# Optimization experiments

Hardware: AMD Instinct MI355X
Metric: run time of the kernel (lower is better)

## Reference

```python
import jax, jax.numpy as jnp
import numpy as np

N = 50000      # total nodes (actors) across batch
E = 300000     # edges surviving the distance threshold
N_AGT = 128    # n_actor
N_CTX = 128    # n_ctx == n_actor for A2A
EPS = 1e-5


def _gn(x, gamma, beta):
    # torch GroupNorm(num_groups=1) on a [N, C] tensor: normalize over C per row
    mu = jnp.mean(x, axis=-1, keepdims=True)
    var = jnp.mean((x - mu) ** 2, axis=-1, keepdims=True)
    return (x - mu) * jax.lax.rsqrt(var + EPS) * gamma + beta


def setup_inputs() -> dict:
    key = jax.random.key(0)
    ks = jax.random.split(key, 16)
    s = 0.02
    f32 = jnp.float32
    inp = {
        'agts': jax.random.normal(ks[0], (N, N_AGT), f32),
        'ctx': jax.random.normal(ks[1], (N, N_CTX), f32),
        'agt_ctrs': jax.random.normal(ks[2], (N, 2), f32),
        'ctx_ctrs': jax.random.normal(ks[3], (N, 2), f32),
        'hi': jax.random.randint(ks[4], (E,), 0, N, dtype=jnp.int32),
        'wi': jax.random.randint(ks[5], (E,), 0, N, dtype=jnp.int32),
        # dist: nn.Linear(2, n_ctx) -> ReLU -> Linear(n_ctx, n_ctx, GN, act)
        'w_d1': jax.random.normal(ks[6], (N_CTX, 2), f32) * s,
        'b_d1': jnp.zeros((N_CTX,), f32),
        'w_d2': jax.random.normal(ks[7], (N_CTX, N_CTX), f32) * s,
        'g_d2': jnp.ones((N_CTX,), f32), 'bt_d2': jnp.zeros((N_CTX,), f32),
        # query: Linear(n_agt, n_ctx, GN, act)
        'w_q': jax.random.normal(ks[8], (N_CTX, N_AGT), f32) * s,
        'g_q': jnp.ones((N_CTX,), f32), 'bt_q': jnp.zeros((N_CTX,), f32),
        # ctx: Linear(3*n_ctx, n_agt, GN, act) -> nn.Linear(n_agt, n_agt, bias=False)
        'w_c1': jax.random.normal(ks[9], (N_AGT, 3 * N_CTX), f32) * s,
        'g_c1': jnp.ones((N_AGT,), f32), 'bt_c1': jnp.zeros((N_AGT,), f32),
        'w_c2': jax.random.normal(ks[10], (N_AGT, N_AGT), f32) * s,
        # agt: nn.Linear(n_agt, n_agt, bias=False)
        'w_a': jax.random.normal(ks[11], (N_AGT, N_AGT), f32) * s,
        # norm: GroupNorm(1, n_agt)
        'g_n': jnp.ones((N_AGT,), f32), 'bt_n': jnp.zeros((N_AGT,), f32),
        # linear: Linear(n_agt, n_agt, GN, act=False)
        'w_l': jax.random.normal(ks[12], (N_AGT, N_AGT), f32) * s,
        'g_l': jnp.ones((N_AGT,), f32), 'bt_l': jnp.zeros((N_AGT,), f32),
    }
    return inp


def reference(agts, ctx, agt_ctrs, ctx_ctrs, hi, wi,
              w_d1, b_d1, w_d2, g_d2, bt_d2,
              w_q, g_q, bt_q,
              w_c1, g_c1, bt_c1, w_c2,
              w_a, g_n, bt_n,
              w_l, g_l, bt_l):
    res = agts
    # edge-wise distance features: [E, 2] -> [E, n_ctx]
    d = agt_ctrs[hi] - ctx_ctrs[wi]
    d = jax.nn.relu(d @ w_d1.T + b_d1)
    d = jax.nn.relu(_gn(d @ w_d2.T, g_d2, bt_d2))
    # edge-wise query from gathered target nodes: [E, n_ctx]
    q = jax.nn.relu(_gn(agts[hi] @ w_q.T, g_q, bt_q))
    # fuse dist/query/context: [E, 3*n_ctx] -> [E, n_agt]
    e = jnp.concatenate([d, q, ctx[wi]], axis=-1)
    e = jax.nn.relu(_gn(e @ w_c1.T, g_c1, bt_c1))
    e = e @ w_c2.T
    # scatter-add messages back to nodes
    out = agts @ w_a.T
    out = out.at[hi].add(e)
    out = jax.nn.relu(_gn(out, g_n, bt_n))
    out = _gn(out @ w_l.T, g_l, bt_l)
    return jax.nn.relu(out + res)
```

## Files before the change

### kernel.cpp

```cpp
#include <hip/hip_runtime.h>
#include <hip/hip_bf16.h>

#define NCH 128
#define EB  32
#define NB  32

typedef __attribute__((ext_vector_type(8))) short bf16x8;
typedef __attribute__((ext_vector_type(4))) float f32x4;

__device__ inline unsigned short f2bf(float v) {
    __hip_bfloat16 h = __float2bfloat16(v);
    return __builtin_bit_cast(unsigned short, h);
}
__device__ inline float bf2f(unsigned short u) {
    return __builtin_bit_cast(float, (unsigned int)u << 16);
}

__device__ inline bf16x8 cvt8(const float* __restrict__ p) {
    bf16x8 r;
#pragma unroll
    for (int i = 0; i < 8; ++i) r[i] = (short)f2bf(p[i]);
    return r;
}

template<bool BF>
__device__ inline bf16x8 load_row8(const void* __restrict__ src, int node, int koff) {
    if constexpr (BF)
        return *(const bf16x8*)((const unsigned short*)src + (size_t)node * NCH + koff);
    else
        return cvt8((const float*)src + (size_t)node * NCH + koff);
}

__global__ __launch_bounds__(256) void convert_weights_kernel(
    const float* __restrict__ w_d2, const float* __restrict__ w_q,
    const float* __restrict__ w_c1, const float* __restrict__ w_c2,
    const float* __restrict__ w_a,  const float* __restrict__ w_l,
    unsigned short* __restrict__ out)
{
    int i = blockIdx.x * 256 + threadIdx.x;
    if (i >= 131072) return;
    const float* src; int off;
    if      (i < 16384)  { src = w_d2; off = i; }
    else if (i < 32768)  { src = w_q;  off = i - 16384; }
    else if (i < 49152)  { int j = i - 32768; src = w_c1; off = (j >> 7) * 384 + (j & 127); }
    else if (i < 65536)  { int j = i - 49152; src = w_c1; off = (j >> 7) * 384 + 128 + (j & 127); }
    else if (i < 81920)  { int j = i - 65536; src = w_c1; off = (j >> 7) * 384 + 256 + (j & 127); }
    else if (i < 98304)  { src = w_c2; off = i - 81920; }
    else if (i < 114688) { src = w_a;  off = i - 98304; }
    else                 { src = w_l;  off = i - 114688; }
    out[i] = f2bf(src[off]);
}

__device__ inline void gemm_k128_lds(const unsigned short* __restrict__ A,
                                     const unsigned short* __restrict__ W,
                                     int lane, int wave, f32x4 (&acc)[2][2])
{
#pragma unroll
    for (int k = 0; k < 4; ++k) {
        const int koff = k * 32 + (lane >> 4) * 8;
        bf16x8 a[2], b[2];
#pragma unroll
        for (int m = 0; m < 2; ++m) {
            int r = m * 16 + (lane & 15);
            int byte = (r * 256 + koff * 2) ^ ((r & 7) << 4);
            a[m] = *(const bf16x8*)((const char*)A + byte);
        }
#pragma unroll
        for (int n = 0; n < 2; ++n) {
            int wr = wave * 32 + n * 16 + (lane & 15);
            b[n] = *(const bf16x8*)(W + (size_t)wr * NCH + koff);
        }
#pragma unroll
        for (int m = 0; m < 2; ++m)
#pragma unroll
            for (int n = 0; n < 2; ++n)
                acc[m][n] = __builtin_amdgcn_mfma_f32_16x16x32_bf16(a[m], b[n], acc[m][n], 0, 0, 0);
    }
}

__device__ inline void gn_frag_stats(const f32x4 (&acc)[2][2],
                                     float (*red_s)[4], float (*red_q)[4],
                                     int t, float (&mu)[2][4], float (&rs)[2][4])
{
    const int lane = t & 63, wave = t >> 6;
    float s[2][4], q[2][4];
#pragma unroll
    for (int m = 0; m < 2; ++m)
#pragma unroll
        for (int j = 0; j < 4; ++j) {
            float sv = acc[m][0][j] + acc[m][1][j];
            float qv = acc[m][0][j] * acc[m][0][j] + acc[m][1][j] * acc[m][1][j];
#pragma unroll
            for (int off = 1; off < 16; off <<= 1) {
                sv += __shfl_xor(sv, off);
                qv += __shfl_xor(qv, off);
            }
            s[m][j] = sv; q[m][j] = qv;
        }
    if ((lane & 15) == 0) {
        const int rg = lane >> 4;
#pragma unroll
        for (int m = 0; m < 2; ++m)
#pragma unroll
            for (int j = 0; j < 4; ++j) {
                int r = m * 16 + rg * 4 + j;
                red_s[r][wave] = s[m][j];
                red_q[r][wave] = q[m][j];
            }
    }
    __syncthreads();
#pragma unroll
    for (int m = 0; m < 2; ++m)
#pragma unroll
        for (int j = 0; j < 4; ++j) {
            int r = m * 16 + ((lane >> 4) << 2) + j;
            float4 sv = *(const float4*)red_s[r];
            float4 qv = *(const float4*)red_q[r];
            float ssum = (sv.x + sv.y) + (sv.z + sv.w);
            float qsum = (qv.x + qv.y) + (qv.z + qv.w);
            float m_  = ssum * (1.f / NCH);
            float var = qsum * (1.f / NCH) - m_ * m_;
            mu[m][j] = m_;
            rs[m][j] = rsqrtf(var + 1e-5f);
        }
}

__device__ inline void gn_pack_store(const f32x4 (&acc)[2][2],
                                     const float (&mu)[2][4], const float (&rs)[2][4],
                                     const float* __restrict__ gamma,
                                     const float* __restrict__ beta,
                                     unsigned short* __restrict__ dst, int t)
{
    const int lane = t & 63, wave = t >> 6;
    const int c0 = wave * 32 + (lane & 15);
    const float g0 = gamma[c0],      b0 = beta[c0];
    const float g1 = gamma[c0 + 16], b1 = beta[c0 + 16];
#pragma unroll
    for (int m = 0; m < 2; ++m)
#pragma unroll
        for (int j = 0; j < 4; ++j) {
            int r = m * 16 + ((lane >> 4) << 2) + j;
            float v0 = fmaxf((acc[m][0][j] - mu[m][j]) * rs[m][j] * g0 + b0, 0.f);
            float v1 = fmaxf((acc[m][1][j] - mu[m][j]) * rs[m][j] * g1 + b1, 0.f);
            unsigned int p0 = f2bf(v0), p1 = f2bf(v1);
            unsigned int o0 = (unsigned int)__shfl_xor((int)p0, 1);
            unsigned int o1 = (unsigned int)__shfl_xor((int)p1, 1);
            if (!(lane & 1)) {
                int cb = c0 * 2;
                int byte0 = (r * 256 + cb) ^ ((r & 7) << 4);
                int byte1 = (r * 256 + cb + 32) ^ ((r & 7) << 4);
                *(unsigned int*)((char*)dst + byte0) = (p0 & 0xffffu) | (o0 << 16);
                *(unsigned int*)((char*)dst + byte1) = (p1 & 0xffffu) | (o1 << 16);
            }
        }
    __syncthreads();
}

__device__ inline void frag_pack_global(const f32x4 (&acc)[2][2],
                                        unsigned short* __restrict__ dst,
                                        int n0, int N, int t)
{
    const int lane = t & 63, wave = t >> 6;
    const int c0 = wave * 32 + (lane & 15);
#pragma unroll
    for (int m = 0; m < 2; ++m)
#pragma unroll
        for (int j = 0; j < 4; ++j) {
            int r = m * 16 + ((lane >> 4) << 2) + j;
            int ng = n0 + r;
            unsigned int p0 = f2bf(acc[m][0][j]);
            unsigned int p1 = f2bf(acc[m][1][j]);
            unsigned int o0 = (unsigned int)__shfl_xor((int)p0, 1);
            unsigned int o1 = (unsigned int)__shfl_xor((int)p1, 1);
            if (!(lane & 1) && ng < N) {
                unsigned int* rowp = (unsigned int*)(dst + (size_t)ng * NCH);
                rowp[c0 >> 1]        = (p0 & 0xffffu) | (o0 << 16);
                rowp[(c0 + 16) >> 1] = (p1 & 0xffffu) | (o1 << 16);
            }
        }
}

__global__ __launch_bounds__(256) void node_prep_kernel(
    const float* __restrict__ agts, const float* __restrict__ ctx,
    const unsigned short* __restrict__ wbf,
    const float* __restrict__ g_q, const float* __restrict__ bt_q,
    float* __restrict__ outbuf,
    unsigned short* __restrict__ pq, unsigned short* __restrict__ px, int N)
{
    const int t = threadIdx.x;
    const int lane = t & 63, wave = t >> 6;
    const int n0 = blockIdx.x * NB;

    __shared__ unsigned short bfQ[NB * NCH];
    __shared__ __align__(16) float red_s[NB][4];
    __shared__ __align__(16) float red_q[NB][4];

    const unsigned short* Wq   = wbf + 16384;
    const unsigned short* Wc1q = wbf + 49152;
    const unsigned short* Wc1x = wbf + 65536;
    const unsigned short* Wa   = wbf + 98304;

    int r0 = n0 + (lane & 15);      if (r0 >= N) r0 = N - 1;
    int r1 = n0 + 16 + (lane & 15); if (r1 >= N) r1 = N - 1;

    const f32x4 z = { 0.f, 0.f, 0.f, 0.f };
    f32x4 accO[2][2] = { { z, z }, { z, z } };
    f32x4 accQ[2][2] = { { z, z }, { z, z } };
#pragma unroll
    for (int k = 0; k < 4; ++k) {
        const int koff = k * 32 + (lane >> 4) * 8;
        bf16x8 a[2], bo[2], bq[2];
        a[0] = load_row8<false>(agts, r0, koff);
        a[1] = load_row8<false>(agts, r1, koff);
#pragma unroll
        for (int n = 0; n < 2; ++n) {
            int wr = wave * 32 + n * 16 + (lane & 15);
            bo[n] = *(const bf16x8*)(Wa + (size_t)wr * NCH + koff);
            bq[n] = *(const bf16x8*)(Wq + (size_t)wr * NCH + koff);
        }
#pragma unroll
        for (int m = 0; m < 2; ++m)
#pragma unroll
            for (int n = 0; n < 2; ++n) {
                accO[m][n] = __builtin_amdgcn_mfma_f32_16x16x32_bf16(a[m], bo[n], accO[m][n], 0, 0, 0);
                accQ[m][n] = __builtin_amdgcn_mfma_f32_16x16x32_bf16(a[m], bq[n], accQ[m][n], 0, 0, 0);
            }
    }
#pragma unroll
    for (int m = 0; m < 2; ++m)
#pragma unroll
        for (int n = 0; n < 2; ++n)
#pragma unroll
            for (int j = 0; j < 4; ++j) {
                int r = m * 16 + ((lane >> 4) << 2) + j;
                int ng = n0 + r;
                if (ng < N)
                    outbuf[(size_t)ng * NCH + wave * 32 + n * 16 + (lane & 15)] = accO[m][n][j];
            }
    float mu[2][4], rs[2][4];
    gn_frag_stats(accQ, red_s, red_q, t, mu, rs);
    gn_pack_store(accQ, mu, rs, g_q, bt_q, bfQ, t);

    f32x4 accPq[2][2] = { { z, z }, { z, z } };
    f32x4 accPx[2][2] = { { z, z }, { z, z } };
#pragma unroll
    for (int k = 0; k < 4; ++k) {
        const int koff = k * 32 + (lane >> 4) * 8;
        bf16x8 aq[2], ax[2], bq2[2], bx[2];
#pragma unroll
        for (int m = 0; m < 2; ++m) {
            int r = m * 16 + (lane & 15);
            int byte = (r * 256 + koff * 2) ^ ((r & 7) << 4);
            aq[m] = *(const bf16x8*)((const char*)bfQ + byte);
        }
        ax[0] = load_row8<false>(ctx, r0, koff);
        ax[1] = load_row8<false>(ctx, r1, koff);
#pragma unroll
        for (int n = 0; n < 2; ++n) {
            int wr = wave * 32 + n * 16 + (lane & 15);
            bq2[n] = *(const bf16x8*)(Wc1q + (size_t)wr * NCH + koff);
            bx[n]  = *(const bf16x8*)(Wc1x + (size_t)wr * NCH + koff);
        }
#pragma unroll
        for (int m = 0; m < 2; ++m)
#pragma unroll
            for (int n = 0; n < 2; ++n) {
                accPq[m][n] = __builtin_amdgcn_mfma_f32_16x16x32_bf16(aq[m], bq2[n], accPq[m][n], 0, 0, 0);
                accPx[m][n] = __builtin_amdgcn_mfma_f32_16x16x32_bf16(ax[m], bx[n], accPx[m][n], 0, 0, 0);
            }
    }
    frag_pack_global(accPq, pq, n0, N, t);
    frag_pack_global(accPx, px, n0, N, t);
}

__global__ __launch_bounds__(256) void edge_kernel_pre(
    const unsigned short* __restrict__ pq, const unsigned short* __restrict__ px,
    const float* __restrict__ agt_ctrs, const float* __restrict__ ctx_ctrs,
    const int* __restrict__ hi, const int* __restrict__ wi,
    const float* __restrict__ w_d1, const float* __restrict__ b_d1,
    const float* __restrict__ g_d2, const float* __restrict__ bt_d2,
    const float* __restrict__ g_c1, const float* __restrict__ bt_c1,
    const unsigned short* __restrict__ wbf,
    float* __restrict__ outbuf, int E)
{
    const int t = threadIdx.x;
    const int lane = t & 63;
    const int wave = t >> 6;
    const int e0 = blockIdx.x * EB;

    __shared__ unsigned short bfD[EB * NCH];
    __shared__ float S[EB][NCH + 4];
    __shared__ __align__(16) float red_s[EB][4];
    __shared__ __align__(16) float red_q[EB][4];
    __shared__ int   sh_h[EB], sh_w[EB];
    __shared__ float sh_dx[EB], sh_dy[EB];

    const unsigned short* Wd2  = wbf;
    const unsigned short* Wc1d = wbf + 32768;
    const unsigned short* Wc2  = wbf + 81920;

    if (t < EB) {
        int e = e0 + t; if (e >= E) e = E - 1;
        int h = hi[e], w = wi[e];
        sh_h[t] = h; sh_w[t] = w;
        sh_dx[t] = agt_ctrs[2 * h]     - ctx_ctrs[2 * w];
        sh_dy[t] = agt_ctrs[2 * h + 1] - ctx_ctrs[2 * w + 1];
    }
    __syncthreads();

    {
        const int r  = t >> 3;
        const int cc = t & 7;
        const int h = sh_h[r], w = sh_w[r];
#pragma unroll
        for (int half = 0; half < 2; ++half) {
            int c8 = (cc + half * 8) * 8;
            bf16x8 aq = load_row8<true>(pq, h, c8);
            bf16x8 ax = load_row8<true>(px, w, c8);
#pragma unroll
            for (int i = 0; i < 8; ++i)
                S[r][c8 + i] = bf2f((unsigned short)aq[i]) + bf2f((unsigned short)ax[i]);
        }
    }
    {
        const int c = t & 127, rh = t >> 7;
        const float wa = w_d1[2 * c], wb = w_d1[2 * c + 1], bb = b_d1[c];
#pragma unroll
        for (int i = 0; i < 16; ++i) {
            int r = rh * 16 + i;
            float v = fmaxf(fmaf(wa, sh_dx[r], fmaf(wb, sh_dy[r], bb)), 0.f);
            unsigned int pv = f2bf(v);
            unsigned int ov = (unsigned int)__shfl_xor((int)pv, 1);
            if (!(c & 1)) {
                int byte = (r * 256 + c * 2) ^ ((r & 7) << 4);
                *(unsigned int*)((char*)bfD + byte) = (pv & 0xffffu) | (ov << 16);
            }
        }
    }
    __syncthreads();

    const f32x4 z = { 0.f, 0.f, 0.f, 0.f };
    f32x4 acc[2][2];
    float mu[2][4], rs[2][4];

    acc[0][0] = z; acc[0][1] = z; acc[1][0] = z; acc[1][1] = z;
    gemm_k128_lds(bfD, Wd2, lane, wave, acc);
    gn_frag_stats(acc, red_s, red_q, t, mu, rs);
    gn_pack_store(acc, mu, rs, g_d2, bt_d2, bfD, t);

    acc[0][0] = z; acc[0][1] = z; acc[1][0] = z; acc[1][1] = z;
    gemm_k128_lds(bfD, Wc1d, lane, wave, acc);
    {
        const int c0 = wave * 32 + (lane & 15);
#pragma unroll
        for (int m = 0; m < 2; ++m)
#pragma unroll
            for (int j = 0; j < 4; ++j) {
                int r = m * 16 + ((lane >> 4) << 2) + j;
                acc[m][0][j] += S[r][c0];
                acc[m][1][j] += S[r][c0 + 16];
            }
    }
    gn_frag_stats(acc, red_s, red_q, t, mu, rs);
    gn_pack_store(acc, mu, rs, g_c1, bt_c1, bfD, t);

    acc[0][0] = z; acc[0][1] = z; acc[1][0] = z; acc[1][1] = z;
    gemm_k128_lds(bfD, Wc2, lane, wave, acc);
#pragma unroll
    for (int m = 0; m < 2; ++m)
#pragma unroll
        for (int n = 0; n < 2; ++n)
#pragma unroll
            for (int j = 0; j < 4; ++j) {
                int r = m * 16 + ((lane >> 4) << 2) + j;
                if (e0 + r < E)
                    atomicAdd(&outbuf[(size_t)sh_h[r] * NCH + wave * 32 + n * 16 + (lane & 15)],
                              acc[m][n][j]);
            }
}

__global__ __launch_bounds__(256) void edge_kernel_fb(
    const float* __restrict__ agts, const float* __restrict__ ctx,
    const float* __restrict__ agt_ctrs, const float* __restrict__ ctx_ctrs,
    const int* __restrict__ hi, const int* __restrict__ wi,
    const float* __restrict__ w_d1, const float* __restrict__ b_d1,
    const float* __restrict__ g_d2, const float* __restrict__ bt_d2,
    const float* __restrict__ g_q, const float* __restrict__ bt_q,
    const float* __restrict__ g_c1, const float* __restrict__ bt_c1,
    const unsigned short* __restrict__ wbf,
    float* __restrict__ outbuf, int E)
{
    const int t = threadIdx.x;
    const int lane = t & 63;
    const int wave = t >> 6;
    const int e0 = blockIdx.x * EB;

    __shared__ unsigned short bfQ[EB * NCH];
    __shared__ unsigned short bfD[EB * NCH];
    __shared__ unsigned short bfX[EB * NCH];
    __shared__ __align__(16) float red_s[EB][4];
    __shared__ __align__(16) float red_q[EB][4];
    __shared__ int   sh_h[EB], sh_w[EB];
    __shared__ float sh_dx[EB], sh_dy[EB];

    const unsigned short* Wd2 = wbf;
    const unsigned short* Wq  = wbf + 16384;
    const unsigned short* Wc1d = wbf + 32768;
    const unsigned short* Wc1q = wbf + 49152;
    const unsigned short* Wc1x = wbf + 65536;
    const unsigned short* Wc2 = wbf + 81920;

    if (t < EB) {
        int e = e0 + t; if (e >= E) e = E - 1;
        int h = hi[e], w = wi[e];
        sh_h[t] = h; sh_w[t] = w;
        sh_dx[t] = agt_ctrs[2 * h]     - ctx_ctrs[2 * w];
        sh_dy[t] = agt_ctrs[2 * h + 1] - ctx_ctrs[2 * w + 1];
    }
    __syncthreads();
    {
        const int r  = t >> 3;
        const int cc = t & 7;
        const int h = sh_h[r], w = sh_w[r];
#pragma unroll
        for (int half = 0; half < 2; ++half) {
            int c = cc + half * 8;
            bf16x8 qv = load_row8<false>(agts, h, c * 8);
            bf16x8 xv = load_row8<false>(ctx, w, c * 8);
            int byte = (r * 256 + c * 16) ^ ((r & 7) << 4);
            *(bf16x8*)((char*)bfQ + byte) = qv;
            *(bf16x8*)((char*)bfX + byte) = xv;
        }
    }
    {
        const int c = t & 127, rh = t >> 7;
        const float wa = w_d1[2 * c], wb = w_d1[2 * c + 1], bb = b_d1[c];
#pragma unroll
        for (int i = 0; i < 16; ++i) {
            int r = rh * 16 + i;
            float v = fmaxf(fmaf(wa, sh_dx[r], fmaf(wb, sh_dy[r], bb)), 0.f);
            unsigned int pv = f2bf(v);
            unsigned int ov = (unsigned int)__shfl_xor((int)pv, 1);
            if (!(c & 1)) {
                int byte = (r * 256 + c * 2) ^ ((r & 7) << 4);
                *(unsigned int*)((char*)bfD + byte) = (pv & 0xffffu) | (ov << 16);
            }
        }
    }
    __syncthreads();

    const f32x4 z = { 0.f, 0.f, 0.f, 0.f };
    f32x4 acc[2][2];
    float mu[2][4], rs[2][4];

    acc[0][0] = z; acc[0][1] = z; acc[1][0] = z; acc[1][1] = z;
    gemm_k128_lds(bfD, Wd2, lane, wave, acc);
    gn_frag_stats(acc, red_s, red_q, t, mu, rs);
    gn_pack_store(acc, mu, rs, g_d2, bt_d2, bfD, t);

    acc[0][0] = z; acc[0][1] = z; acc[1][0] = z; acc[1][1] = z;
    gemm_k128_lds(bfQ, Wq, lane, wave, acc);
    gn_frag_stats(acc, red_s, red_q, t, mu, rs);
    gn_pack_store(acc, mu, rs, g_q, bt_q, bfQ, t);

    acc[0][0] = z; acc[0][1] = z; acc[1][0] = z; acc[1][1] = z;
    gemm_k128_lds(bfD, Wc1d, lane, wave, acc);
    gemm_k128_lds(bfQ, Wc1q, lane, wave, acc);
    gemm_k128_lds(bfX, Wc1x, lane, wave, acc);
    gn_frag_stats(acc, red_s, red_q, t, mu, rs);
    gn_pack_store(acc, mu, rs, g_c1, bt_c1, bfD, t);

    acc[0][0] = z; acc[0][1] = z; acc[1][0] = z; acc[1][1] = z;
    gemm_k128_lds(bfD, Wc2, lane, wave, acc);
#pragma unroll
    for (int m = 0; m < 2; ++m)
#pragma unroll
        for (int n = 0; n < 2; ++n)
#pragma unroll
            for (int j = 0; j < 4; ++j) {
                int r = m * 16 + ((lane >> 4) << 2) + j;
                if (e0 + r < E)
                    atomicAdd(&outbuf[(size_t)sh_h[r] * NCH + wave * 32 + n * 16 + (lane & 15)],
                              acc[m][n][j]);
            }
}

__global__ __launch_bounds__(256) void node_init_kernel(
    const float* __restrict__ agts, const unsigned short* __restrict__ wa_bf,
    float* __restrict__ outbuf, int N)
{
    const int t = threadIdx.x;
    const int lane = t & 63, wave = t >> 6;
    const int n0 = blockIdx.x * NB;

    int r0 = n0 + (lane & 15);      if (r0 >= N) r0 = N - 1;
    int r1 = n0 + 16 + (lane & 15); if (r1 >= N) r1 = N - 1;

    const f32x4 z = { 0.f, 0.f, 0.f, 0.f };
    f32x4 acc[2][2] = { { z, z }, { z, z } };
#pragma unroll
    for (int k = 0; k < 4; ++k) {
        const int koff = k * 32 + (lane >> 4) * 8;
        bf16x8 a[2], b[2];
        a[0] = load_row8<false>(agts, r0, koff);
        a[1] = load_row8<false>(agts, r1, koff);
#pragma unroll
        for (int n = 0; n < 2; ++n) {
            int wr = wave * 32 + n * 16 + (lane & 15);
            b[n] = *(const bf16x8*)(wa_bf + (size_t)wr * NCH + koff);
        }
#pragma unroll
        for (int m = 0; m < 2; ++m)
#pragma unroll
            for (int n = 0; n < 2; ++n)
                acc[m][n] = __builtin_amdgcn_mfma_f32_16x16x32_bf16(a[m], b[n], acc[m][n], 0, 0, 0);
    }
#pragma unroll
    for (int m = 0; m < 2; ++m)
#pragma unroll
        for (int n = 0; n < 2; ++n)
#pragma unroll
            for (int j = 0; j < 4; ++j) {
                int r = m * 16 + ((lane >> 4) << 2) + j;
                int ng = n0 + r;
                if (ng < N)
                    outbuf[(size_t)ng * NCH + wave * 32 + n * 16 + (lane & 15)] = acc[m][n][j];
            }
}

__global__ __launch_bounds__(256) void node_post_kernel(
    float* __restrict__ outbuf, const float* __restrict__ agts,
    const float* __restrict__ g_n, const float* __restrict__ bt_n,
    const unsigned short* __restrict__ wl_bf,
    const float* __restrict__ g_l, const float* __restrict__ bt_l, int N)
{
    const int t = threadIdx.x;
    const int lane = t & 63, wave = t >> 6;
    const int n0 = blockIdx.x * NB;

    __shared__ unsigned short bfP[NB * NCH];
    __shared__ __align__(16) float red_s[NB][4];
    __shared__ __align__(16) float red_q[NB][4];

    const int c = t & 127, rh = t >> 7;
    float v[16];
#pragma unroll
    for (int i = 0; i < 16; ++i) {
        int n = n0 + rh * 16 + i; if (n >= N) n = N - 1;
        v[i] = outbuf[(size_t)n * NCH + c];
    }
#pragma unroll
    for (int i = 0; i < 16; ++i) {
        float s = v[i], q = v[i] * v[i];
        for (int off = 32; off > 0; off >>= 1) {
            s += __shfl_down(s, off);
            q += __shfl_down(q, off);
        }
        if (lane == 0) { red_s[rh * 16 + i][wave & 1] = s; red_q[rh * 16 + i][wave & 1] = q; }
    }
    __syncthreads();
    {
        const float g = g_n[c], b = bt_n[c];
#pragma unroll
        for (int i = 0; i < 16; ++i) {
            int r = rh * 16 + i;
            float s = red_s[r][0] + red_s[r][1];
            float q = red_q[r][0] + red_q[r][1];
            float m_  = s * (1.f / NCH);
            float var = q * (1.f / NCH) - m_ * m_;
            float rrs = rsqrtf(var + 1e-5f);
            float val = fmaxf((v[i] - m_) * rrs * g + b, 0.f);
            unsigned int pv = f2bf(val);
            unsigned int ov = (unsigned int)__shfl_xor((int)pv, 1);
            if (!(c & 1)) {
                int byte = (r * 256 + c * 2) ^ ((r & 7) << 4);
                *(unsigned int*)((char*)bfP + byte) = (pv & 0xffffu) | (ov << 16);
            }
        }
    }
    __syncthreads();

    const f32x4 z = { 0.f, 0.f, 0.f, 0.f };
    f32x4 acc[2][2] = { { z, z }, { z, z } };
    gemm_k128_lds(bfP, wl_bf, lane, wave, acc);

    float mu[2][4], rs[2][4];
    gn_frag_stats(acc, red_s, red_q, t, mu, rs);
    const int c0 = wave * 32 + (lane & 15);
    const float g0 = g_l[c0],      b0 = bt_l[c0];
    const float g1 = g_l[c0 + 16], b1 = bt_l[c0 + 16];
#pragma unroll
    for (int m = 0; m < 2; ++m)
#pragma unroll
        for (int j = 0; j < 4; ++j) {
            int r = m * 16 + ((lane >> 4) << 2) + j;
            int ng = n0 + r;
            if (ng < N) {
                float v0 = (acc[m][0][j] - mu[m][j]) * rs[m][j] * g0 + b0;
                float v1 = (acc[m][1][j] - mu[m][j]) * rs[m][j] * g1 + b1;
                v0 = fmaxf(v0 + agts[(size_t)ng * NCH + c0], 0.f);
                v1 = fmaxf(v1 + agts[(size_t)ng * NCH + c0 + 16], 0.f);
                outbuf[(size_t)ng * NCH + c0]      = v0;
                outbuf[(size_t)ng * NCH + c0 + 16] = v1;
            }
        }
}

extern "C" void kernel_launch(void* const* d_in, const int* in_sizes, int n_in,
                              void* d_out, int out_size, void* d_ws, size_t ws_size,
                              hipStream_t stream) {
    const float* agts     = (const float*)d_in[0];
    const float* ctx      = (const float*)d_in[1];
    const float* agt_ctrs = (const float*)d_in[2];
    const float* ctx_ctrs = (const float*)d_in[3];
    const int*   hi       = (const int*)d_in[4];
    const int*   wi       = (const int*)d_in[5];
    const float* w_d1     = (const float*)d_in[6];
    const float* b_d1     = (const float*)d_in[7];
    const float* w_d2     = (const float*)d_in[8];
    const float* g_d2     = (const float*)d_in[9];
    const float* bt_d2    = (const float*)d_in[10];
    const float* w_q      = (const float*)d_in[11];
    const float* g_q      = (const float*)d_in[12];
    const float* bt_q     = (const float*)d_in[13];
    const float* w_c1     = (const float*)d_in[14];
    const float* g_c1     = (const float*)d_in[15];
    const float* bt_c1    = (const float*)d_in[16];
    const float* w_c2     = (const float*)d_in[17];
    const float* w_a      = (const float*)d_in[18];
    const float* g_n      = (const float*)d_in[19];
    const float* bt_n     = (const float*)d_in[20];
    const float* w_l      = (const float*)d_in[21];
    const float* g_l      = (const float*)d_in[22];
    const float* bt_l     = (const float*)d_in[23];

    const int N = in_sizes[0] / NCH;
    const int E = in_sizes[4];

    float* outbuf = (float*)d_out;

    unsigned short* wbf = (unsigned short*)d_ws;
    unsigned short* pq  = wbf + 131072;
    unsigned short* px  = pq + (size_t)N * NCH;
    const size_t need = 262144ull + (size_t)N * NCH * 4ull;
    const bool big = (d_ws != nullptr) && (ws_size >= need);

    const int nb_nodes = (N + NB - 1) / NB;
    const int nb_edges = (E + EB - 1) / EB;

    convert_weights_kernel<<<512, 256, 0, stream>>>(w_d2, w_q, w_c1, w_c2, w_a, w_l, wbf);

    if (big) {
        node_prep_kernel<<<nb_nodes, 256, 0, stream>>>(
            agts, ctx, wbf, g_q, bt_q, outbuf, pq, px, N);
        edge_kernel_pre<<<nb_edges, 256, 0, stream>>>(
            pq, px, agt_ctrs, ctx_ctrs, hi, wi,
            w_d1, b_d1, g_d2, bt_d2, g_c1, bt_c1,
            wbf, outbuf, E);
    } else {
        node_init_kernel<<<nb_nodes, 256, 0, stream>>>(agts, wbf + 98304, outbuf, N);
        edge_kernel_fb<<<nb_edges, 256, 0, stream>>>(
            agts, ctx, agt_ctrs, ctx_ctrs, hi, wi,
            w_d1, b_d1, g_d2, bt_d2, g_q, bt_q, g_c1, bt_c1,
            wbf, outbuf, E);
    }
    node_post_kernel<<<nb_nodes, 256, 0, stream>>>(
        outbuf, agts, g_n, bt_n, wbf + 114688, g_l, bt_l, N);
}
```

Measured before the change: 308.9 us.

## Give each wave its own 16 edge rows and drop block barriers

The precomputed edge kernel now gives each wave 16 full edge rows across all 128 output columns, so each block covers 64 edges instead of 32. GroupNorm statistics are reduced within the wave using shuffles instead of shared-memory reductions, and block-wide __syncthreads calls become wave-local LDS waits. B-operand weights are read straight from global memory (L2/L1) rather than through the shared helper. This cuts barrier and reduction overhead and halves the block count, at the cost of more accumulator registers per wave and more global weight traffic.

```diff
diff --git a/kernel.cpp b/kernel.cpp
--- a/kernel.cpp
+++ b/kernel.cpp
@@ -2,7 +2,7 @@
 #include <hip/hip_bf16.h>
 
 #define NCH 128
-#define EB  32
+#define EB  64
 #define NB  32
 
 typedef __attribute__((ext_vector_type(8))) short bf16x8;
@@ -29,6 +29,10 @@
         return *(const bf16x8*)((const unsigned short*)src + (size_t)node * NCH + koff);
     else
         return cvt8((const float*)src + (size_t)node * NCH + koff);
+}
+
+__device__ inline void lds_fence() {
+    asm volatile("s_waitcnt lgkmcnt(0)" ::: "memory");
 }
 
 __global__ __launch_bounds__(256) void convert_weights_kernel(
@@ -287,96 +291,194 @@
     const int lane = t & 63;
     const int wave = t >> 6;
     const int e0 = blockIdx.x * EB;
+    const int row0 = wave * 16;
 
     __shared__ unsigned short bfD[EB * NCH];
     __shared__ float S[EB][NCH + 4];
-    __shared__ __align__(16) float red_s[EB][4];
-    __shared__ __align__(16) float red_q[EB][4];
-    __shared__ int   sh_h[EB], sh_w[EB];
-    __shared__ float sh_dx[EB], sh_dy[EB];
 
     const unsigned short* Wd2  = wbf;
     const unsigned short* Wc1d = wbf + 32768;
     const unsigned short* Wc2  = wbf + 81920;
 
-    if (t < EB) {
-        int e = e0 + t; if (e >= E) e = E - 1;
-        int h = hi[e], w = wi[e];
-        sh_h[t] = h; sh_w[t] = w;
-        sh_dx[t] = agt_ctrs[2 * h]     - ctx_ctrs[2 * w];
-        sh_dy[t] = agt_ctrs[2 * h + 1] - ctx_ctrs[2 * w + 1];
-    }
-    __syncthreads();
-
+    int hval = 0, wval = 0;
+    float dxval = 0.f, dyval = 0.f;
     {
-        const int r  = t >> 3;
-        const int cc = t & 7;
-        const int h = sh_h[r], w = sh_w[r];
-#pragma unroll
-        for (int half = 0; half < 2; ++half) {
-            int c8 = (cc + half * 8) * 8;
+        int e = e0 + row0 + (lane & 15); if (e >= E) e = E - 1;
+        if (lane < 16) {
+            hval = hi[e]; wval = wi[e];
+            dxval = agt_ctrs[2 * hval]     - ctx_ctrs[2 * wval];
+            dyval = agt_ctrs[2 * hval + 1] - ctx_ctrs[2 * wval + 1];
+        }
+    }
+
+    {
+        const int rl = lane >> 2;
+        const int qq = lane & 3;
+        const int h = __shfl(hval, rl);
+        const int w = __shfl(wval, rl);
+        const int r = row0 + rl;
+#pragma unroll
+        for (int i = 0; i < 4; ++i) {
+            int c8 = qq * 32 + i * 8;
             bf16x8 aq = load_row8<true>(pq, h, c8);
             bf16x8 ax = load_row8<true>(px, w, c8);
-#pragma unroll
-            for (int i = 0; i < 8; ++i)
-                S[r][c8 + i] = bf2f((unsigned short)aq[i]) + bf2f((unsigned short)ax[i]);
+            float4 lo, hi4;
+            lo.x = bf2f((unsigned short)aq[0]) + bf2f((unsigned short)ax[0]);
+            lo.y = bf2f((unsigned short)aq[1]) + bf2f((unsigned short)ax[1]);
+            lo.z = bf2f((unsigned short)aq[2]) + bf2f((unsigned short)ax[2]);
+            lo.w = bf2f((unsigned short)aq[3]) + bf2f((unsigned short)ax[3]);
+            hi4.x = bf2f((unsigned short)aq[4]) + bf2f((unsigned short)ax[4]);
+            hi4.y = bf2f((unsigned short)aq[5]) + bf2f((unsigned short)ax[5]);
+            hi4.z = bf2f((unsigned short)aq[6]) + bf2f((unsigned short)ax[6]);
+            hi4.w = bf2f((unsigned short)aq[7]) + bf2f((unsigned short)ax[7]);
+            *(float4*)&S[r][c8]     = lo;
+            *(float4*)&S[r][c8 + 4] = hi4;
         }
     }
     {
-        const int c = t & 127, rh = t >> 7;
-        const float wa = w_d1[2 * c], wb = w_d1[2 * c + 1], bb = b_d1[c];
-#pragma unroll
-        for (int i = 0; i < 16; ++i) {
-            int r = rh * 16 + i;
-            float v = fmaxf(fmaf(wa, sh_dx[r], fmaf(wb, sh_dy[r], bb)), 0.f);
-            unsigned int pv = f2bf(v);
-            unsigned int ov = (unsigned int)__shfl_xor((int)pv, 1);
-            if (!(c & 1)) {
-                int byte = (r * 256 + c * 2) ^ ((r & 7) << 4);
-                *(unsigned int*)((char*)bfD + byte) = (pv & 0xffffu) | (ov << 16);
-            }
-        }
-    }
-    __syncthreads();
+        const int rl = lane & 15;
+        const int r = row0 + rl;
+        const float dx = __shfl(dxval, rl);
+        const float dy = __shfl(dyval, rl);
+#pragma unroll
+        for (int cc = 0; cc < 4; ++cc) {
+            const int c0 = (lane >> 4) * 8 + cc * 32;
+            uint4 packed;
+            unsigned int* pp = (unsigned int*)&packed;
+#pragma unroll
+            for (int p = 0; p < 4; ++p) {
+                int c = c0 + p * 2;
+                float4 wv = *(const float4*)&w_d1[2 * c];
+                float b0 = b_d1[c], b1 = b_d1[c + 1];
+                float v0 = fmaxf(fmaf(wv.x, dx, fmaf(wv.y, dy, b0)), 0.f);
+                float v1 = fmaxf(fmaf(wv.z, dx, fmaf(wv.w, dy, b1)), 0.f);
+                pp[p] = (unsigned int)f2bf(v0) | ((unsigned int)f2bf(v1) << 16);
+            }
+            int byte = (r * 256 + c0 * 2) ^ ((r & 7) << 4);
+            *(uint4*)((char*)bfD + byte) = packed;
+        }
+    }
+    lds_fence();
 
     const f32x4 z = { 0.f, 0.f, 0.f, 0.f };
-    f32x4 acc[2][2];
-    float mu[2][4], rs[2][4];
-
-    acc[0][0] = z; acc[0][1] = z; acc[1][0] = z; acc[1][1] = z;
-    gemm_k128_lds(bfD, Wd2, lane, wave, acc);
-    gn_frag_stats(acc, red_s, red_q, t, mu, rs);
-    gn_pack_store(acc, mu, rs, g_d2, bt_d2, bfD, t);
-
-    acc[0][0] = z; acc[0][1] = z; acc[1][0] = z; acc[1][1] = z;
-    gemm_k128_lds(bfD, Wc1d, lane, wave, acc);
+    const int ar = row0 + (lane & 15);
+    const int abase = (lane >> 4) * 8;
+    const int cl = lane & 15;
+    float mu[4], rsx[4];
+
+    f32x4 acc[8];
+
+#pragma unroll
+    for (int n = 0; n < 8; ++n) acc[n] = z;
+#pragma unroll
+    for (int k = 0; k < 4; ++k) {
+        const int koff = k * 32 + abase;
+        bf16x8 a = *(const bf16x8*)((const char*)bfD + ((ar * 256 + koff * 2) ^ ((ar & 7) << 4)));
+#pragma unroll
+        for (int n = 0; n < 8; ++n) {
+            bf16x8 b = *(const bf16x8*)(Wd2 + (size_t)(n * 16 + cl) * NCH + koff);
+            acc[n] = __builtin_amdgcn_mfma_f32_16x16x32_bf16(a, b, acc[n], 0, 0, 0);
+        }
+    }
+#pragma unroll
+    for (int j = 0; j < 4; ++j) {
+        float s = 0.f, q = 0.f;
+#pragma unroll
+        for (int n = 0; n < 8; ++n) { float v = acc[n][j]; s += v; q += v * v; }
+#pragma unroll
+        for (int off = 1; off < 16; off <<= 1) { s += __shfl_xor(s, off); q += __shfl_xor(q, off); }
+        float m_ = s * (1.f / NCH);
+        float var = q * (1.f / NCH) - m_ * m_;
+        mu[j] = m_; rsx[j] = rsqrtf(var + 1e-5f);
+    }
     {
-        const int c0 = wave * 32 + (lane & 15);
-#pragma unroll
-        for (int m = 0; m < 2; ++m)
-#pragma unroll
-            for (int j = 0; j < 4; ++j) {
-                int r = m * 16 + ((lane >> 4) << 2) + j;
-                acc[m][0][j] += S[r][c0];
-                acc[m][1][j] += S[r][c0 + 16];
-            }
-    }
-    gn_frag_stats(acc, red_s, red_q, t, mu, rs);
-    gn_pack_store(acc, mu, rs, g_c1, bt_c1, bfD, t);
-
-    acc[0][0] = z; acc[0][1] = z; acc[1][0] = z; acc[1][1] = z;
-    gemm_k128_lds(bfD, Wc2, lane, wave, acc);
-#pragma unroll
-    for (int m = 0; m < 2; ++m)
-#pragma unroll
-        for (int n = 0; n < 2; ++n)
-#pragma unroll
-            for (int j = 0; j < 4; ++j) {
-                int r = m * 16 + ((lane >> 4) << 2) + j;
-                if (e0 + r < E)
-                    atomicAdd(&outbuf[(size_t)sh_h[r] * NCH + wave * 32 + n * 16 + (lane & 15)],
-                              acc[m][n][j]);
-            }
+#pragma unroll
+        for (int j = 0; j < 4; ++j) {
+            int r = row0 + ((lane >> 4) << 2) + j;
+#pragma unroll
+            for (int n = 0; n < 8; ++n) {
+                int c = n * 16 + cl;
+                float v = fmaxf((acc[n][j] - mu[j]) * rsx[j] * g_d2[c] + bt_d2[c], 0.f);
+                unsigned int p = f2bf(v);
+                unsigned int o = (unsigned int)__shfl_xor((int)p, 1);
+                if (!(lane & 1)) {
+                    int byte = (r * 256 + c * 2) ^ ((r & 7) << 4);
+                    *(unsigned int*)((char*)bfD + byte) = (p & 0xffffu) | (o << 16);
+                }
+            }
+        }
+    }
+    lds_fence();
+
+#pragma unroll
+    for (int j = 0; j < 4; ++j) {
+        int r = row0 + ((lane >> 4) << 2) + j;
+#pragma unroll
+        for (int n = 0; n < 8; ++n) acc[n][j] = S[r][n * 16 + cl];
+    }
+#pragma unroll
+    for (int k = 0; k < 4; ++k) {
+        const int koff = k * 32 + abase;
+        bf16x8 a = *(const bf16x8*)((const char*)bfD + ((ar * 256 + koff * 2) ^ ((ar & 7) << 4)));
+#pragma unroll
+        for (int n = 0; n < 8; ++n) {
+            bf16x8 b = *(const bf16x8*)(Wc1d + (size_t)(n * 16 + cl) * NCH + koff);
+            acc[n] = __builtin_amdgcn_mfma_f32_16x16x32_bf16(a, b, acc[n], 0, 0, 0);
+        }
+    }
+#pragma unroll
+    for (int j = 0; j < 4; ++j) {
+        float s = 0.f, q = 0.f;
+#pragma unroll
+        for (int n = 0; n < 8; ++n) { float v = acc[n][j]; s += v; q += v * v; }
+#pragma unroll
+        for (int off = 1; off < 16; off <<= 1) { s += __shfl_xor(s, off); q += __shfl_xor(q, off); }
+        float m_ = s * (1.f / NCH);
+        float var = q * (1.f / NCH) - m_ * m_;
+        mu[j] = m_; rsx[j] = rsqrtf(var + 1e-5f);
+    }
+    {
+#pragma unroll
+        for (int j = 0; j < 4; ++j) {
+            int r = row0 + ((lane >> 4) << 2) + j;
+#pragma unroll
+            for (int n = 0; n < 8; ++n) {
+                int c = n * 16 + cl;
+                float v = fmaxf((acc[n][j] - mu[j]) * rsx[j] * g_c1[c] + bt_c1[c], 0.f);
+                unsigned int p = f2bf(v);
+                unsigned int o = (unsigned int)__shfl_xor((int)p, 1);
+                if (!(lane & 1)) {
+                    int byte = (r * 256 + c * 2) ^ ((r & 7) << 4);
+                    *(unsigned int*)((char*)bfD + byte) = (p & 0xffffu) | (o << 16);
+                }
+            }
+        }
+    }
+    lds_fence();
+
+#pragma unroll
+    for (int n = 0; n < 8; ++n) acc[n] = z;
+#pragma unroll
+    for (int k = 0; k < 4; ++k) {
+        const int koff = k * 32 + abase;
+        bf16x8 a = *(const bf16x8*)((const char*)bfD + ((ar * 256 + koff * 2) ^ ((ar & 7) << 4)));
+#pragma unroll
+        for (int n = 0; n < 8; ++n) {
+            bf16x8 b = *(const bf16x8*)(Wc2 + (size_t)(n * 16 + cl) * NCH + koff);
+            acc[n] = __builtin_amdgcn_mfma_f32_16x16x32_bf16(a, b, acc[n], 0, 0, 0);
+        }
+    }
+#pragma unroll
+    for (int j = 0; j < 4; ++j) {
+        int rl = ((lane >> 4) << 2) + j;
+        int e = e0 + row0 + rl;
+        int h = __shfl(hval, rl);
+        if (e < E) {
+#pragma unroll
+            for (int n = 0; n < 8; ++n)
+                atomicAdd(&outbuf[(size_t)h * NCH + n * 16 + cl], acc[n][j]);
+        }
+    }
 }
 
 __global__ __launch_bounds__(256) void edge_kernel_fb(
@@ -393,15 +495,15 @@
     const int t = threadIdx.x;
     const int lane = t & 63;
     const int wave = t >> 6;
-    const int e0 = blockIdx.x * EB;
-
-    __shared__ unsigned short bfQ[EB * NCH];
-    __shared__ unsigned short bfD[EB * NCH];
-    __shared__ unsigned short bfX[EB * NCH];
-    __shared__ __align__(16) float red_s[EB][4];
-    __shared__ __align__(16) float red_q[EB][4];
-    __shared__ int   sh_h[EB], sh_w[EB];
-    __shared__ float sh_dx[EB], sh_dy[EB];
+    const int e0 = blockIdx.x * 32;
+
+    __shared__ unsigned short bfQ[32 * NCH];
+    __shared__ unsigned short bfD[32 * NCH];
+    __shared__ unsigned short bfX[32 * NCH];
+    __shared__ __align__(16) float red_s[32][4];
+    __shared__ __align__(16) float red_q[32][4];
+    __shared__ int   sh_h[32], sh_w[32];
+    __shared__ float sh_dx[32], sh_dy[32];
 
     const unsigned short* Wd2 = wbf;
     const unsigned short* Wq  = wbf + 16384;
@@ -410,7 +512,7 @@
     const unsigned short* Wc1x = wbf + 65536;
     const unsigned short* Wc2 = wbf + 81920;
 
-    if (t < EB) {
+    if (t < 32) {
         int e = e0 + t; if (e >= E) e = E - 1;
         int h = hi[e], w = wi[e];
         sh_h[t] = h; sh_w[t] = w;
@@ -646,20 +748,19 @@
     const bool big = (d_ws != nullptr) && (ws_size >= need);
 
     const int nb_nodes = (N + NB - 1) / NB;
-    const int nb_edges = (E + EB - 1) / EB;
 
     convert_weights_kernel<<<512, 256, 0, stream>>>(w_d2, w_q, w_c1, w_c2, w_a, w_l, wbf);
 
     if (big) {
         node_prep_kernel<<<nb_nodes, 256, 0, stream>>>(
             agts, ctx, wbf, g_q, bt_q, outbuf, pq, px, N);
-        edge_kernel_pre<<<nb_edges, 256, 0, stream>>>(
+        edge_kernel_pre<<<(E + EB - 1) / EB, 256, 0, stream>>>(
             pq, px, agt_ctrs, ctx_ctrs, hi, wi,
             w_d1, b_d1, g_d2, bt_d2, g_c1, bt_c1,
             wbf, outbuf, E);
     } else {
         node_init_kernel<<<nb_nodes, 256, 0, stream>>>(agts, wbf + 98304, outbuf, N);
-        edge_kernel_fb<<<nb_edges, 256, 0, stream>>>(
+        edge_kernel_fb<<<(E + 31) / 32, 256, 0, stream>>>(
             agts, ctx, agt_ctrs, ctx_ctrs, hi, wi,
             w_d1, b_d1, g_d2, bt_d2, g_q, bt_q, g_c1, bt_c1,
             wbf, outbuf, E);
```

Measured after the change: 455.6 us. 47.5% more time.

## Process 64 edges per block with dual-accumulator GEMMs reusing weight fragments

Applied to the files above, without the earlier changes.

Doubles the per-block edge tile in the precomputed edge kernel from 32 to 64 rows. Each wave now loads each weight fragment once and feeds two MFMA accumulator sets covering both 32-row halves, which halves weight traffic per edge and raises MFMA density. The c1 GEMM is seeded directly with the precomputed q+x sums, and the S staging uses float4 stores. The cost is higher register pressure, roughly double the LDS per block, and fewer blocks in the grid, which may lower occupancy.

```diff
diff --git a/kernel.cpp b/kernel.cpp
--- a/kernel.cpp
+++ b/kernel.cpp
@@ -2,7 +2,7 @@
 #include <hip/hip_bf16.h>
 
 #define NCH 128
-#define EB  32
+#define EB  64
 #define NB  32
 
 typedef __attribute__((ext_vector_type(8))) short bf16x8;
@@ -78,36 +78,121 @@
     }
 }
 
+__device__ inline void gemm_k128_dual(const unsigned short* __restrict__ A,
+                                      const unsigned short* __restrict__ W,
+                                      int lane, int wave,
+                                      f32x4 (&accA)[2][2], f32x4 (&accB)[2][2])
+{
+#pragma unroll
+    for (int k = 0; k < 4; ++k) {
+        const int koff = k * 32 + (lane >> 4) * 8;
+        bf16x8 b[2];
+#pragma unroll
+        for (int n = 0; n < 2; ++n) {
+            int wr = wave * 32 + n * 16 + (lane & 15);
+            b[n] = *(const bf16x8*)(W + (size_t)wr * NCH + koff);
+        }
+        bf16x8 a0[2], a1[2];
+#pragma unroll
+        for (int m = 0; m < 2; ++m) {
+            int r = m * 16 + (lane & 15);
+            a0[m] = *(const bf16x8*)((const char*)A + ((r * 256 + koff * 2) ^ ((r & 7) << 4)));
+            int r2 = r + 32;
+            a1[m] = *(const bf16x8*)((const char*)A + ((r2 * 256 + koff * 2) ^ ((r2 & 7) << 4)));
+        }
+#pragma unroll
+        for (int m = 0; m < 2; ++m)
+#pragma unroll
+            for (int n = 0; n < 2; ++n) {
+                accA[m][n] = __builtin_amdgcn_mfma_f32_16x16x32_bf16(a0[m], b[n], accA[m][n], 0, 0, 0);
+                accB[m][n] = __builtin_amdgcn_mfma_f32_16x16x32_bf16(a1[m], b[n], accB[m][n], 0, 0, 0);
+            }
+    }
+}
+
+__device__ inline void gn_stats_half(const f32x4 (&acc)[2][2],
+                                     float (*red_s)[4], float (*red_q)[4],
+                                     int lane, int wave, int roff)
+{
+#pragma unroll
+    for (int m = 0; m < 2; ++m)
+#pragma unroll
+        for (int j = 0; j < 4; ++j) {
+            float sv = acc[m][0][j] + acc[m][1][j];
+            float qv = acc[m][0][j] * acc[m][0][j] + acc[m][1][j] * acc[m][1][j];
+#pragma unroll
+            for (int off = 1; off < 16; off <<= 1) {
+                sv += __shfl_xor(sv, off);
+                qv += __shfl_xor(qv, off);
+            }
+            if ((lane & 15) == 0) {
+                int r = roff + m * 16 + (lane >> 4) * 4 + j;
+                red_s[r][wave] = sv;
+                red_q[r][wave] = qv;
+            }
+        }
+}
+
+__device__ inline void gn_apply_half(const f32x4 (&acc)[2][2],
+                                     float (*red_s)[4], float (*red_q)[4],
+                                     const float* __restrict__ gamma,
+                                     const float* __restrict__ beta,
+                                     unsigned short* __restrict__ dst,
+                                     int lane, int wave, int roff)
+{
+    const int c0 = wave * 32 + (lane & 15);
+    const float g0 = gamma[c0],      b0 = beta[c0];
+    const float g1 = gamma[c0 + 16], b1 = beta[c0 + 16];
+#pragma unroll
+    for (int m = 0; m < 2; ++m)
+#pragma unroll
+        for (int j = 0; j < 4; ++j) {
+            int r = roff + m * 16 + ((lane >> 4) << 2) + j;
+            float4 sv = *(const float4*)red_s[r];
+            float4 qv = *(const float4*)red_q[r];
+            float ssum = (sv.x + sv.y) + (sv.z + sv.w);
+            float qsum = (qv.x + qv.y) + (qv.z + qv.w);
+            float mu  = ssum * (1.f / NCH);
+            float var = qsum * (1.f / NCH) - mu * mu;
+            float rs  = rsqrtf(var + 1e-5f);
+            float v0 = fmaxf((acc[m][0][j] - mu) * rs * g0 + b0, 0.f);
+            float v1 = fmaxf((acc[m][1][j] - mu) * rs * g1 + b1, 0.f);
+            unsigned int p0 = f2bf(v0), p1 = f2bf(v1);
+            unsigned int o0 = (unsigned int)__shfl_xor((int)p0, 1);
+            unsigned int o1 = (unsigned int)__shfl_xor((int)p1, 1);
+            if (!(lane & 1)) {
+                int cb = c0 * 2;
+                int byte0 = (r * 256 + cb) ^ ((r & 7) << 4);
+                int byte1 = (r * 256 + cb + 32) ^ ((r & 7) << 4);
+                *(unsigned int*)((char*)dst + byte0) = (p0 & 0xffffu) | (o0 << 16);
+                *(unsigned int*)((char*)dst + byte1) = (p1 & 0xffffu) | (o1 << 16);
+            }
+        }
+}
+
+__device__ inline void scatter_half(const f32x4 (&acc)[2][2], const int* __restrict__ sh_h,
+                                    float* __restrict__ outbuf, int e0, int E,
+                                    int lane, int wave, int roff)
+{
+#pragma unroll
+    for (int m = 0; m < 2; ++m)
+#pragma unroll
+        for (int n = 0; n < 2; ++n)
+#pragma unroll
+            for (int j = 0; j < 4; ++j) {
+                int r = roff + m * 16 + ((lane >> 4) << 2) + j;
+                if (e0 + r < E)
+                    atomicAdd(&outbuf[(size_t)sh_h[r] * NCH + wave * 32 + n * 16 + (lane & 15)],
+                              acc[m][n][j]);
+            }
+}
+
 __device__ inline void gn_frag_stats(const f32x4 (&acc)[2][2],
                                      float (*red_s)[4], float (*red_q)[4],
                                      int t, float (&mu)[2][4], float (&rs)[2][4])
 {
     const int lane = t & 63, wave = t >> 6;
-    float s[2][4], q[2][4];
-#pragma unroll
-    for (int m = 0; m < 2; ++m)
-#pragma unroll
-        for (int j = 0; j < 4; ++j) {
-            float sv = acc[m][0][j] + acc[m][1][j];
-            float qv = acc[m][0][j] * acc[m][0][j] + acc[m][1][j] * acc[m][1][j];
-#pragma unroll
-            for (int off = 1; off < 16; off <<= 1) {
-                sv += __shfl_xor(sv, off);
-                qv += __shfl_xor(qv, off);
-            }
-            s[m][j] = sv; q[m][j] = qv;
-        }
-    if ((lane & 15) == 0) {
-        const int rg = lane >> 4;
-#pragma unroll
-        for (int m = 0; m < 2; ++m)
-#pragma unroll
-            for (int j = 0; j < 4; ++j) {
-                int r = m * 16 + rg * 4 + j;
-                red_s[r][wave] = s[m][j];
-                red_q[r][wave] = q[m][j];
-            }
-    }
+    gn_stats_half(acc, red_s, red_q, lane, wave, 0);
     __syncthreads();
 #pragma unroll
     for (int m = 0; m < 2; ++m)
@@ -309,25 +394,33 @@
     __syncthreads();
 
     {
-        const int r  = t >> 3;
-        const int cc = t & 7;
+        const int r  = t >> 2;
+        const int q4 = t & 3;
         const int h = sh_h[r], w = sh_w[r];
 #pragma unroll
-        for (int half = 0; half < 2; ++half) {
-            int c8 = (cc + half * 8) * 8;
+        for (int i = 0; i < 4; ++i) {
+            int c8 = (q4 * 4 + i) * 8;
             bf16x8 aq = load_row8<true>(pq, h, c8);
             bf16x8 ax = load_row8<true>(px, w, c8);
-#pragma unroll
-            for (int i = 0; i < 8; ++i)
-                S[r][c8 + i] = bf2f((unsigned short)aq[i]) + bf2f((unsigned short)ax[i]);
+            float4 lo, hi4;
+            lo.x = bf2f((unsigned short)aq[0]) + bf2f((unsigned short)ax[0]);
+            lo.y = bf2f((unsigned short)aq[1]) + bf2f((unsigned short)ax[1]);
+            lo.z = bf2f((unsigned short)aq[2]) + bf2f((unsigned short)ax[2]);
+            lo.w = bf2f((unsigned short)aq[3]) + bf2f((unsigned short)ax[3]);
+            hi4.x = bf2f((unsigned short)aq[4]) + bf2f((unsigned short)ax[4]);
+            hi4.y = bf2f((unsigned short)aq[5]) + bf2f((unsigned short)ax[5]);
+            hi4.z = bf2f((unsigned short)aq[6]) + bf2f((unsigned short)ax[6]);
+            hi4.w = bf2f((unsigned short)aq[7]) + bf2f((unsigned short)ax[7]);
+            *(float4*)&S[r][c8]     = lo;
+            *(float4*)&S[r][c8 + 4] = hi4;
         }
     }
     {
         const int c = t & 127, rh = t >> 7;
         const float wa = w_d1[2 * c], wb = w_d1[2 * c + 1], bb = b_d1[c];
 #pragma unroll
-        for (int i = 0; i < 16; ++i) {
-            int r = rh * 16 + i;
+        for (int i = 0; i < 32; ++i) {
+            int r = rh * 32 + i;
             float v = fmaxf(fmaf(wa, sh_dx[r], fmaf(wb, sh_dy[r], bb)), 0.f);
             unsigned int pv = f2bf(v);
             unsigned int ov = (unsigned int)__shfl_xor((int)pv, 1);
@@ -340,16 +433,18 @@
     __syncthreads();
 
     const f32x4 z = { 0.f, 0.f, 0.f, 0.f };
-    f32x4 acc[2][2];
-    float mu[2][4], rs[2][4];
-
-    acc[0][0] = z; acc[0][1] = z; acc[1][0] = z; acc[1][1] = z;
-    gemm_k128_lds(bfD, Wd2, lane, wave, acc);
-    gn_frag_stats(acc, red_s, red_q, t, mu, rs);
-    gn_pack_store(acc, mu, rs, g_d2, bt_d2, bfD, t);
-
-    acc[0][0] = z; acc[0][1] = z; acc[1][0] = z; acc[1][1] = z;
-    gemm_k128_lds(bfD, Wc1d, lane, wave, acc);
+    f32x4 accA[2][2], accB[2][2];
+
+    accA[0][0] = z; accA[0][1] = z; accA[1][0] = z; accA[1][1] = z;
+    accB[0][0] = z; accB[0][1] = z; accB[1][0] = z; accB[1][1] = z;
+    gemm_k128_dual(bfD, Wd2, lane, wave, accA, accB);
+    gn_stats_half(accA, red_s, red_q, lane, wave, 0);
+    gn_stats_half(accB, red_s, red_q, lane, wave, 32);
+    __syncthreads();
+    gn_apply_half(accA, red_s, red_q, g_d2, bt_d2, bfD, lane, wave, 0);
+    gn_apply_half(accB, red_s, red_q, g_d2, bt_d2, bfD, lane, wave, 32);
+    __syncthreads();
+
     {
         const int c0 = wave * 32 + (lane & 15);
 #pragma unroll
@@ -357,26 +452,23 @@
 #pragma unroll
             for (int j = 0; j < 4; ++j) {
                 int r = m * 16 + ((lane >> 4) << 2) + j;
-                acc[m][0][j] += S[r][c0];
-                acc[m][1][j] += S[r][c0 + 16];
-            }
-    }
-    gn_frag_stats(acc, red_s, red_q, t, mu, rs);
-    gn_pack_store(acc, mu, rs, g_c1, bt_c1, bfD, t);
-
-    acc[0][0] = z; acc[0][1] = z; acc[1][0] = z; acc[1][1] = z;
-    gemm_k128_lds(bfD, Wc2, lane, wave, acc);
-#pragma unroll
-    for (int m = 0; m < 2; ++m)
-#pragma unroll
-        for (int n = 0; n < 2; ++n)
-#pragma unroll
-            for (int j = 0; j < 4; ++j) {
-                int r = m * 16 + ((lane >> 4) << 2) + j;
-                if (e0 + r < E)
-                    atomicAdd(&outbuf[(size_t)sh_h[r] * NCH + wave * 32 + n * 16 + (lane & 15)],
-                              acc[m][n][j]);
-            }
+                accA[m][0][j] = S[r][c0];      accA[m][1][j] = S[r][c0 + 16];
+                accB[m][0][j] = S[r + 32][c0]; accB[m][1][j] = S[r + 32][c0 + 16];
+            }
+    }
+    gemm_k128_dual(bfD, Wc1d, lane, wave, accA, accB);
+    gn_stats_half(accA, red_s, red_q, lane, wave, 0);
+    gn_stats_half(accB, red_s, red_q, lane, wave, 32);
+    __syncthreads();
+    gn_apply_half(accA, red_s, red_q, g_c1, bt_c1, bfD, lane, wave, 0);
+    gn_apply_half(accB, red_s, red_q, g_c1, bt_c1, bfD, lane, wave, 32);
+    __syncthreads();
+
+    accA[0][0] = z; accA[0][1] = z; accA[1][0] = z; accA[1][1] = z;
+    accB[0][0] = z; accB[0][1] = z; accB[1][0] = z; accB[1][1] = z;
+    gemm_k128_dual(bfD, Wc2, lane, wave, accA, accB);
+    scatter_half(accA, sh_h, outbuf, e0, E, lane, wave, 0);
+    scatter_half(accB, sh_h, outbuf, e0, E, lane, wave, 32);
 }
 
 __global__ __launch_bounds__(256) void edge_kernel_fb(
@@ -393,15 +485,15 @@
     const int t = threadIdx.x;
     const int lane = t & 63;
     const int wave = t >> 6;
-    const int e0 = blockIdx.x * EB;
-
-    __shared__ unsigned short bfQ[EB * NCH];
-    __shared__ unsigned short bfD[EB * NCH];
-    __shared__ unsigned short bfX[EB * NCH];
-    __shared__ __align__(16) float red_s[EB][4];
-    __shared__ __align__(16) float red_q[EB][4];
-    __shared__ int   sh_h[EB], sh_w[EB];
-    __shared__ float sh_dx[EB], sh_dy[EB];
+    const int e0 = blockIdx.x * 32;
+
+    __shared__ unsigned short bfQ[32 * NCH];
+    __shared__ unsigned short bfD[32 * NCH];
+    __shared__ unsigned short bfX[32 * NCH];
+    __shared__ __align__(16) float red_s[32][4];
+    __shared__ __align__(16) float red_q[32][4];
+    __shared__ int   sh_h[32], sh_w[32];
+    __shared__ float sh_dx[32], sh_dy[32];
 
     const unsigned short* Wd2 = wbf;
     const unsigned short* Wq  = wbf + 16384;
@@ -410,7 +502,7 @@
     const unsigned short* Wc1x = wbf + 65536;
     const unsigned short* Wc2 = wbf + 81920;
 
-    if (t < EB) {
+    if (t < 32) {
         int e = e0 + t; if (e >= E) e = E - 1;
         int h = hi[e], w = wi[e];
         sh_h[t] = h; sh_w[t] = w;
@@ -646,20 +738,19 @@
     const bool big = (d_ws != nullptr) && (ws_size >= need);
 
     const int nb_nodes = (N + NB - 1) / NB;
-    const int nb_edges = (E + EB - 1) / EB;
 
     convert_weights_kernel<<<512, 256, 0, stream>>>(w_d2, w_q, w_c1, w_c2, w_a, w_l, wbf);
 
     if (big) {
         node_prep_kernel<<<nb_nodes, 256, 0, stream>>>(
             agts, ctx, wbf, g_q, bt_q, outbuf, pq, px, N);
-        edge_kernel_pre<<<nb_edges, 256, 0, stream>>>(
+        edge_kernel_pre<<<(E + EB - 1) / EB, 256, 0, stream>>>(
             pq, px, agt_ctrs, ctx_ctrs, hi, wi,
             w_d1, b_d1, g_d2, bt_d2, g_c1, bt_c1,
             wbf, outbuf, E);
     } else {
         node_init_kernel<<<nb_nodes, 256, 0, stream>>>(agts, wbf + 98304, outbuf, N);
-        edge_kernel_fb<<<nb_edges, 256, 0, stream>>>(
+        edge_kernel_fb<<<(E + 31) / 32, 256, 0, stream>>>(
             agts, ctx, agt_ctrs, ctx_ctrs, hi, wi,
             w_d1, b_d1, g_d2, bt_d2, g_q, bt_q, g_c1, bt_c1,
             wbf, outbuf, E);
```

After: 305.4 us (median of 2 runs). About the same (-1.1%).
